# Kernel optimization log

Measured on AMD Instinct MI355X. Metric: run time of the kernel, lower is better.

## Reference

```python
import jax, jax.numpy as jnp
import numpy as np

UAV_DIM, TASK_DIM = 32, 32
E, H, HID = 128, 4, 256
B, U, T = 16, 64, 128
ENC_H = 128  # encoder hidden width


def _mlp3(x, w0, b0, w1, b1, w2, b2):
    # Linear->ReLU->Linear->ReLU->Linear (weights stored as (in,out))
    x = jax.nn.relu(x @ w0 + b0)
    x = jax.nn.relu(x @ w1 + b1)
    return x @ w2 + b2


def setup_inputs() -> dict:
    key = jax.random.key(0)
    ks = jax.random.split(key, 20)
    s = lambda fan_in: 1.0 / np.sqrt(fan_in)
    d = {
        'uav_feat': jax.random.normal(ks[0], (B, U, UAV_DIM), jnp.float32),
        'task_feat': jax.random.normal(ks[1], (B, T, TASK_DIM), jnp.float32),
        # UAV encoder
        'uw0': jax.random.normal(ks[2], (UAV_DIM, ENC_H), jnp.float32) * s(UAV_DIM),
        'ub0': jnp.zeros((ENC_H,), jnp.float32),
        'uw1': jax.random.normal(ks[3], (ENC_H, ENC_H), jnp.float32) * s(ENC_H),
        'ub1': jnp.zeros((ENC_H,), jnp.float32),
        'uw2': jax.random.normal(ks[4], (ENC_H, E), jnp.float32) * s(ENC_H),
        'ub2': jnp.zeros((E,), jnp.float32),
        # Task encoder
        'tw0': jax.random.normal(ks[5], (TASK_DIM, ENC_H), jnp.float32) * s(TASK_DIM),
        'tb0': jnp.zeros((ENC_H,), jnp.float32),
        'tw1': jax.random.normal(ks[6], (ENC_H, ENC_H), jnp.float32) * s(ENC_H),
        'tb1': jnp.zeros((ENC_H,), jnp.float32),
        'tw2': jax.random.normal(ks[7], (ENC_H, E), jnp.float32) * s(ENC_H),
        'tb2': jnp.zeros((E,), jnp.float32),
        # head queries + fusion MLP (fw1 is the (2E,HID) first linear)
        'head_q': jax.random.normal(ks[8], (H, E), jnp.float32),
        'fw1': jax.random.normal(ks[9], (2 * E, HID), jnp.float32) * s(2 * E),
        'fb1': jnp.zeros((HID,), jnp.float32),
        'fw2': jax.random.normal(ks[10], (HID, 1), jnp.float32) * s(HID),
        'fb2': jnp.zeros((1,), jnp.float32),
    }
    return d


def reference(uav_feat, task_feat, uw0, ub0, uw1, ub1, uw2, ub2,
              tw0, tb0, tw1, tb1, tw2, tb2, head_q, fw1, fb1, fw2, fb2):
    ue = _mlp3(uav_feat, uw0, ub0, uw1, ub1, uw2, ub2)   # (B,U,E)
    te = _mlp3(task_feat, tw0, tb0, tw1, tb1, tw2, tb2)  # (B,T,E)
    # q = uav_embed + per-head query: (B,H,U,E)
    q = ue[:, None, :, :] + head_q[None, :, None, :]
    # Split cat([q,k]) @ fw1 into q@fw1[:E] + k@fw1[E:] — same math, no 2E concat
    qh = jnp.einsum('bhue,ed->bhud', q, fw1[:E])          # (B,H,U,HID)
    kh = jnp.einsum('bte,ed->btd', te, fw1[E:])           # (B,T,HID)
    pre = qh[:, :, :, None, :] + kh[:, None, None, :, :] + fb1  # (B,H,U,T,HID)
    h = jax.nn.relu(pre)
    logits = jnp.einsum('bhutd,do->bhuto', h, fw2)[..., 0] + fb2[0]  # (B,H,U,T)
    return logits
```

## Files before the change

### kernel.cpp

```cpp
#include <hip/hip_runtime.h>
#include <hip/hip_bf16.h>

#define B_ 16
#define U_ 64
#define T_ 128
#define H_ 4
#define E_ 128
#define HID_ 256

typedef _Float16 half_t;
typedef _Float16 h2 __attribute__((ext_vector_type(2)));
typedef _Float16 f16x8 __attribute__((ext_vector_type(8)));
typedef float f32x4 __attribute__((ext_vector_type(4)));

__device__ __forceinline__ h2 u2h(unsigned u){ h2 r; __builtin_memcpy(&r, &u, 4); return r; }
__device__ __forceinline__ unsigned pkh(float a, float b){
  h2 r; r.x = (_Float16)a; r.y = (_Float16)b;
  unsigned u; __builtin_memcpy(&u, &r, 4); return u;
}

__global__ __launch_bounds__(256) void prep_kernel(
  const float* __restrict__ uw0, const float* __restrict__ uw1, const float* __restrict__ uw2,
  const float* __restrict__ tw0, const float* __restrict__ tw1, const float* __restrict__ tw2,
  const float* __restrict__ fw1, const float* __restrict__ headq,
  half_t* __restrict__ u0t, half_t* __restrict__ u1t, half_t* __restrict__ u2t,
  half_t* __restrict__ t0t, half_t* __restrict__ t1t, half_t* __restrict__ t2t,
  half_t* __restrict__ f1at, half_t* __restrict__ f1bt, float* __restrict__ QhW)
{
  const int tid = threadIdx.x;
  const int b = blockIdx.x;
  if (b == 34) {
    const int n = tid;
    float acc[4] = {0.f,0.f,0.f,0.f};
    for (int e=0;e<128;e++){
      float w = fw1[e*256 + n];
      #pragma unroll
      for (int h=0;h<4;h++) acc[h] = fmaf(headq[h*128+e], w, acc[h]);
    }
    #pragma unroll
    for (int h=0;h<4;h++) QhW[h*256+n] = acc[h];
    return;
  }
  const float* src; int srcStride, row0, col0; half_t* dst; int dstStride, nOff, kOff;
  if (b < 9) {
    if (b==0){ src=uw0; row0=0;        dst=u0t; dstStride=32;  kOff=0; }
    else if (b<5){ src=uw1; row0=(b-1)*32; dst=u1t; dstStride=128; kOff=row0; }
    else { src=uw2; row0=(b-5)*32; dst=u2t; dstStride=128; kOff=row0; }
    srcStride=128; col0=0; nOff=0;
  } else if (b < 18) {
    int bb=b-9;
    if (bb==0){ src=tw0; row0=0;        dst=t0t; dstStride=32;  kOff=0; }
    else if (bb<5){ src=tw1; row0=(bb-1)*32; dst=t1t; dstStride=128; kOff=row0; }
    else { src=tw2; row0=(bb-5)*32; dst=t2t; dstStride=128; kOff=row0; }
    srcStride=128; col0=0; nOff=0;
  } else if (b < 26) {
    int idx=b-18, kc=idx&3, nc=idx>>2;
    src=fw1; srcStride=256; row0=kc*32; col0=nc*128;
    dst=f1at; dstStride=128; kOff=kc*32; nOff=col0;
  } else {
    int idx=b-26, kc=idx&3, nc=idx>>2;
    src=fw1; srcStride=256; row0=128+kc*32; col0=nc*128;
    dst=f1bt; dstStride=128; kOff=kc*32; nOff=col0;
  }
  __shared__ half_t tl[128][33];
  #pragma unroll
  for (int i=0;i<16;i++){ int idx=i*256+tid; int k=idx>>7, n=idx&127;
    tl[n][k] = (half_t)src[(row0+k)*srcStride + col0 + n]; }
  __syncthreads();
  #pragma unroll
  for (int i=0;i<16;i++){ int idx=i*256+tid; int n=idx>>5, k=idx&31;
    dst[(nOff+n)*dstStride + kOff + k] = tl[n][k]; }
}

#define PITCH 136

template<int KTILES, int NTILES, bool RELU>
__device__ __forceinline__ void layer_mfma(const half_t* __restrict__ in,
    const half_t* __restrict__ W, const float* __restrict__ bias,
    half_t* __restrict__ out, int m0, int quad, int l16)
{
  f16x8 bfrag[KTILES];
  const half_t* ip = in + (m0+l16)*PITCH + quad*8;
  #pragma unroll
  for (int kk=0;kk<KTILES;kk++) bfrag[kk] = *(const f16x8*)(ip + kk*32);
  #pragma unroll
  for (int nt=0; nt<NTILES; nt++){
    f32x4 acc = {0.f,0.f,0.f,0.f};
    const half_t* wp = W + (nt*16+l16)*PITCH + quad*8;
    #pragma unroll
    for (int kk=0;kk<KTILES;kk++){
      f16x8 a = *(const f16x8*)(wp + kk*32);
      acc = __builtin_amdgcn_mfma_f32_16x16x32_f16(a, bfrag[kk], acc, 0, 0, 0);
    }
    const int n0 = nt*16 + quad*4;
    const float4 bv = *(const float4*)(bias + n0);
    float bvr[4] = {bv.x, bv.y, bv.z, bv.w};
    union { half_t h[4]; uint2 u; } pv;
    #pragma unroll
    for (int r=0;r<4;r++){
      float x = acc[r] + bvr[r];
      if (RELU) x = fmaxf(x, 0.f);
      pv.h[r] = (half_t)x;
    }
    *(uint2*)(out + (m0+l16)*PITCH + n0) = pv.u;
  }
}

__global__ __launch_bounds__(256) void enc_mfma(
  const float* __restrict__ uav, const float* __restrict__ task,
  const float* __restrict__ ub0, const float* __restrict__ ub1, const float* __restrict__ ub2,
  const float* __restrict__ tb0, const float* __restrict__ tb1, const float* __restrict__ tb2,
  const half_t* __restrict__ u0t, const half_t* __restrict__ u1t, const half_t* __restrict__ u2t,
  const half_t* __restrict__ t0t, const half_t* __restrict__ t1t, const half_t* __restrict__ t2t,
  const half_t* __restrict__ f1at, const half_t* __restrict__ f1bt,
  float* __restrict__ ueW, half_t* __restrict__ Kg)
{
  __shared__ half_t Wb[256*PITCH];
  __shared__ half_t actA[64*PITCH];
  __shared__ half_t actB[64*PITCH];
  const int tid = threadIdx.x, lane = tid&63, wv = tid>>6;
  const int quad = lane>>4, l16 = lane&15;
  const int m0 = wv*16;
  const bool isU = blockIdx.x < 16;
  const int rows0 = (isU ? blockIdx.x : blockIdx.x - 16) * 64;
  const float* Xsrc = (isU ? uav : task) + rows0*32;
  const half_t* W0 = isU ? u0t : t0t;
  const half_t* W1 = isU ? u1t : t1t;
  const half_t* W2 = isU ? u2t : t2t;
  const half_t* W3 = isU ? f1at : f1bt;
  const float* bias0 = isU ? ub0 : tb0;
  const float* bias1 = isU ? ub1 : tb1;
  const float* bias2 = isU ? ub2 : tb2;

  {
    const int r = tid>>2, q = tid&3;
    const float4 v0 = *(const float4*)(Xsrc + r*32 + q*8);
    const float4 v1 = *(const float4*)(Xsrc + r*32 + q*8 + 4);
    half_t* d = actA + r*PITCH + q*8;
    d[0]=(half_t)v0.x; d[1]=(half_t)v0.y; d[2]=(half_t)v0.z; d[3]=(half_t)v0.w;
    d[4]=(half_t)v1.x; d[5]=(half_t)v1.y; d[6]=(half_t)v1.z; d[7]=(half_t)v1.w;
  }
  {
    const uint4* s = (const uint4*)W0;
    #pragma unroll
    for (int i=0;i<2;i++){ int idx=i*256+tid; int n=idx>>2, kc=idx&3;
      *(uint4*)(Wb + n*PITCH + kc*8) = s[idx]; }
  }
  __syncthreads();
  layer_mfma<1,8,true >(actA, Wb, bias0, actB, m0, quad, l16);
  __syncthreads();
  { const uint4* s = (const uint4*)W1;
    #pragma unroll
    for (int i=0;i<8;i++){ int idx=i*256+tid; int n=idx>>4, kc=idx&15;
      *(uint4*)(Wb + n*PITCH + kc*8) = s[idx]; } }
  __syncthreads();
  layer_mfma<4,8,true >(actB, Wb, bias1, actA, m0, quad, l16);
  __syncthreads();
  { const uint4* s = (const uint4*)W2;
    #pragma unroll
    for (int i=0;i<8;i++){ int idx=i*256+tid; int n=idx>>4, kc=idx&15;
      *(uint4*)(Wb + n*PITCH + kc*8) = s[idx]; } }
  __syncthreads();
  layer_mfma<4,8,false>(actA, Wb, bias2, actB, m0, quad, l16);
  __syncthreads();
  { const uint4* s = (const uint4*)W3;
    #pragma unroll
    for (int i=0;i<16;i++){ int idx=i*256+tid; int n=idx>>4, kc=idx&15;
      *(uint4*)(Wb + n*PITCH + kc*8) = s[idx]; } }
  __syncthreads();
  {
    f16x8 bfrag[4];
    const half_t* ip = actB + (m0+l16)*PITCH + quad*8;
    #pragma unroll
    for (int kk=0;kk<4;kk++) bfrag[kk] = *(const f16x8*)(ip + kk*32);
    const int grow = rows0 + m0 + l16;
    #pragma unroll
    for (int nt=0; nt<16; nt++){
      f32x4 acc = {0.f,0.f,0.f,0.f};
      const half_t* wp = Wb + (nt*16+l16)*PITCH + quad*8;
      #pragma unroll
      for (int kk=0;kk<4;kk++){
        f16x8 a = *(const f16x8*)(wp + kk*32);
        acc = __builtin_amdgcn_mfma_f32_16x16x32_f16(a, bfrag[kk], acc, 0, 0, 0);
      }
      const int n0 = nt*16 + quad*4;
      if (isU){
        *(float4*)(ueW + grow*256 + n0) = make_float4(acc[0],acc[1],acc[2],acc[3]);
      } else {
        union { half_t h[4]; uint2 u; } pv;
        pv.h[0]=(half_t)acc[0]; pv.h[1]=(half_t)acc[1];
        pv.h[2]=(half_t)acc[2]; pv.h[3]=(half_t)acc[3];
        *(uint2*)(Kg + grow*256 + n0) = pv.u;
      }
    }
  }
}

#define UTILE 8

__global__ __launch_bounds__(256) void logits_kernel(
  const float* __restrict__ ueW, const float* __restrict__ QhW,
  const half_t* __restrict__ Kg,
  const float* __restrict__ fb1, const float* __restrict__ fw2,
  const float* __restrict__ fb2, float* __restrict__ out)
{
  __shared__ uint4 Kl4[64*32];
  __shared__ uint4 baseb[UTILE][32];
  __shared__ uint4 w2b[32];

  const int tid = threadIdx.x;
  const int wv = tid >> 6;
  const int lane = tid & 63;
  const int b = blockIdx.z, h = blockIdx.y;
  const int u0 = blockIdx.x * UTILE;

  {
    const int u = tid >> 5;
    const int c = tid & 31;
    const float4* ue4 = (const float4*)(ueW + (b*U_ + u0 + u)*HID_);
    const float4* q4  = (const float4*)(QhW + h*HID_);
    const float4* f4  = (const float4*)fb1;
    float4 a0 = ue4[2*c],   a1 = ue4[2*c+1];
    float4 b0 = q4[2*c],    b1 = q4[2*c+1];
    float4 c0 = f4[2*c],    c1 = f4[2*c+1];
    uint4 pv;
    pv.x = pkh(a0.x+b0.x+c0.x, a0.y+b0.y+c0.y);
    pv.y = pkh(a0.z+b0.z+c0.z, a0.w+b0.w+c0.w);
    pv.z = pkh(a1.x+b1.x+c1.x, a1.y+b1.y+c1.y);
    pv.w = pkh(a1.z+b1.z+c1.z, a1.w+b1.w+c1.w);
    baseb[u][c] = pv;
    if (tid < 32) {
      const float4* w4 = (const float4*)fw2;
      float4 w0 = w4[2*tid], w1 = w4[2*tid+1];
      uint4 wv4;
      wv4.x = pkh(w0.x, w0.y); wv4.y = pkh(w0.z, w0.w);
      wv4.z = pkh(w1.x, w1.y); wv4.w = pkh(w1.z, w1.w);
      w2b[tid] = wv4;
    }
  }
  const float fb2f = fb2[0];
  const uint4* Kgp = (const uint4*)(Kg + (size_t)b*T_*HID_);

  const int r0 = wv*2;
  const h2 hz = (h2)((_Float16)0);

  for (int s=0; s<2; s++){
    const int t0 = s*64;
    if (s) __syncthreads();
    for (int i = tid; i < 64*32; i += 256){
      const int t = i >> 5, c = i & 31;
      Kl4[t*32 + ((c + t)&31)] = Kgp[(t0 + t)*32 + c];
    }
    __syncthreads();
    const uint4* myrow = Kl4 + lane*32;
    float acc0 = 0.f, acc1 = 0.f;
    #pragma unroll
    for (int c=0; c<32; c++){
      const uint4 kv = myrow[(c + lane)&31];
      const uint4 w4 = w2b[c];
      const uint4 p0 = baseb[r0][c];
      const uint4 p1 = baseb[r0+1][c];
      h2 x;
      x = __builtin_elementwise_max(u2h(p0.x)+u2h(kv.x), hz);
      acc0 = __builtin_amdgcn_fdot2(x, u2h(w4.x), acc0, false);
      x = __builtin_elementwise_max(u2h(p0.y)+u2h(kv.y), hz);
      acc0 = __builtin_amdgcn_fdot2(x, u2h(w4.y), acc0, false);
      x = __builtin_elementwise_max(u2h(p0.z)+u2h(kv.z), hz);
      acc0 = __builtin_amdgcn_fdot2(x, u2h(w4.z), acc0, false);
      x = __builtin_elementwise_max(u2h(p0.w)+u2h(kv.w), hz);
      acc0 = __builtin_amdgcn_fdot2(x, u2h(w4.w), acc0, false);
      x = __builtin_elementwise_max(u2h(p1.x)+u2h(kv.x), hz);
      acc1 = __builtin_amdgcn_fdot2(x, u2h(w4.x), acc1, false);
      x = __builtin_elementwise_max(u2h(p1.y)+u2h(kv.y), hz);
      acc1 = __builtin_amdgcn_fdot2(x, u2h(w4.y), acc1, false);
      x = __builtin_elementwise_max(u2h(p1.z)+u2h(kv.z), hz);
      acc1 = __builtin_amdgcn_fdot2(x, u2h(w4.z), acc1, false);
      x = __builtin_elementwise_max(u2h(p1.w)+u2h(kv.w), hz);
      acc1 = __builtin_amdgcn_fdot2(x, u2h(w4.w), acc1, false);
    }
    const int t = t0 + lane;
    out[((b*H_ + h)*U_ + (u0 + r0    ))*T_ + t] = acc0 + fb2f;
    out[((b*H_ + h)*U_ + (u0 + r0 + 1))*T_ + t] = acc1 + fb2f;
  }
}

extern "C" void kernel_launch(void* const* d_in, const int* in_sizes, int n_in,
                              void* d_out, int out_size, void* d_ws, size_t ws_size,
                              hipStream_t stream)
{
  const float* uav  = (const float*)d_in[0];
  const float* task = (const float*)d_in[1];
  const float* uw0=(const float*)d_in[2];  const float* ub0=(const float*)d_in[3];
  const float* uw1=(const float*)d_in[4];  const float* ub1=(const float*)d_in[5];
  const float* uw2=(const float*)d_in[6];  const float* ub2=(const float*)d_in[7];
  const float* tw0=(const float*)d_in[8];  const float* tb0=(const float*)d_in[9];
  const float* tw1=(const float*)d_in[10]; const float* tb1=(const float*)d_in[11];
  const float* tw2=(const float*)d_in[12]; const float* tb2=(const float*)d_in[13];
  const float* headq=(const float*)d_in[14];
  const float* fw1=(const float*)d_in[15];
  const float* fb1=(const float*)d_in[16];
  const float* fw2=(const float*)d_in[17];
  const float* fb2=(const float*)d_in[18];

  float* ueW = (float*)d_ws;
  float* QhW = ueW + 262144;
  half_t* hb = (half_t*)(QhW + 1024);
  half_t* u0t  = hb;
  half_t* u1t  = hb + 4096;
  half_t* u2t  = hb + 20480;
  half_t* t0t  = hb + 36864;
  half_t* t1t  = hb + 40960;
  half_t* t2t  = hb + 57344;
  half_t* f1at = hb + 73728;
  half_t* f1bt = hb + 106496;
  half_t* Kg   = hb + 139264;

  float* out = (float*)d_out;

  hipLaunchKernelGGL(prep_kernel, dim3(35), dim3(256), 0, stream,
      uw0, uw1, uw2, tw0, tw1, tw2, fw1, headq,
      u0t, u1t, u2t, t0t, t1t, t2t, f1at, f1bt, QhW);
  hipLaunchKernelGGL(enc_mfma, dim3(48), dim3(256), 0, stream,
      uav, task, ub0, ub1, ub2, tb0, tb1, tb2,
      u0t, u1t, u2t, t0t, t1t, t2t, f1at, f1bt, ueW, Kg);
  hipLaunchKernelGGL(logits_kernel, dim3(U_/UTILE, H_, B_), dim3(256), 0, stream,
      ueW, QhW, Kg, fb1, fw2, fb2, out);
}
```

Baseline: 116.1 us.

## Fuse weight prep into encoder kernel and restructure logits tiling

Removes the separate weight-transpose/convert prep kernel; the encoder now reads the fp32 weights directly, converts them to fp16 while staging into shared memory, and computes QhW in an extra block. Weight staging for later layers is overlapped with MFMA compute through fewer barriers and separate buffers. The logits kernel now loads all 128 task rows of K into shared memory at once, and each thread computes 4 u-rows instead of 2 across two passes. The cost is more LDS per block, which may lower occupancy, and strided uncoalesced fp32 weight reads in every encoder block.

```diff
diff --git a/kernel.cpp b/kernel.cpp
--- a/kernel.cpp
+++ b/kernel.cpp
@@ -19,17 +19,76 @@
   unsigned u; __builtin_memcpy(&u, &r, 4); return u;
 }
 
-__global__ __launch_bounds__(256) void prep_kernel(
-  const float* __restrict__ uw0, const float* __restrict__ uw1, const float* __restrict__ uw2,
-  const float* __restrict__ tw0, const float* __restrict__ tw1, const float* __restrict__ tw2,
-  const float* __restrict__ fw1, const float* __restrict__ headq,
-  half_t* __restrict__ u0t, half_t* __restrict__ u1t, half_t* __restrict__ u2t,
-  half_t* __restrict__ t0t, half_t* __restrict__ t1t, half_t* __restrict__ t2t,
-  half_t* __restrict__ f1at, half_t* __restrict__ f1bt, float* __restrict__ QhW)
-{
+#define PITCH 136
+#define PITCH0 40
+
+template<int KC, int SRCN>
+__device__ __forceinline__ void stageW(const float* __restrict__ src,
+    half_t* __restrict__ dst, int n, int kc0, int pitch)
+{
+  #pragma unroll
+  for (int f=0; f<KC; f++){
+    const int kc = kc0 + f;
+    float v[8];
+    #pragma unroll
+    for (int j=0;j<8;j++) v[j] = src[(kc*8+j)*SRCN + n];
+    union{ half_t h[8]; uint4 u; } p;
+    #pragma unroll
+    for (int j=0;j<8;j++) p.h[j] = (half_t)v[j];
+    *(uint4*)(dst + n*pitch + kc*8) = p.u;
+  }
+}
+
+template<int KTILES, int NTILES, int WPITCH, bool RELU>
+__device__ __forceinline__ void layer_mfma(const half_t* __restrict__ in,
+    const half_t* __restrict__ W, const float* __restrict__ bias,
+    half_t* __restrict__ out, int m0, int quad, int l16)
+{
+  f16x8 bfrag[KTILES];
+  const half_t* ip = in + (m0+l16)*PITCH + quad*8;
+  #pragma unroll
+  for (int kk=0;kk<KTILES;kk++) bfrag[kk] = *(const f16x8*)(ip + kk*32);
+  #pragma unroll
+  for (int nt=0; nt<NTILES; nt++){
+    f32x4 acc = {0.f,0.f,0.f,0.f};
+    const half_t* wp = W + (nt*16+l16)*WPITCH + quad*8;
+    #pragma unroll
+    for (int kk=0;kk<KTILES;kk++){
+      f16x8 a = *(const f16x8*)(wp + kk*32);
+      acc = __builtin_amdgcn_mfma_f32_16x16x32_f16(a, bfrag[kk], acc, 0, 0, 0);
+    }
+    const int n0 = nt*16 + quad*4;
+    const float4 bv = *(const float4*)(bias + n0);
+    float bvr[4] = {bv.x, bv.y, bv.z, bv.w};
+    union { half_t h[4]; uint2 u; } pv;
+    #pragma unroll
+    for (int r=0;r<4;r++){
+      float x = acc[r] + bvr[r];
+      if (RELU) x = fmaxf(x, 0.f);
+      pv.h[r] = (half_t)x;
+    }
+    *(uint2*)(out + (m0+l16)*PITCH + n0) = pv.u;
+  }
+}
+
+__global__ __launch_bounds__(256) void enc_mfma(
+  const float* __restrict__ uav, const float* __restrict__ task,
+  const float* __restrict__ uw0, const float* __restrict__ ub0,
+  const float* __restrict__ uw1, const float* __restrict__ ub1,
+  const float* __restrict__ uw2, const float* __restrict__ ub2,
+  const float* __restrict__ tw0, const float* __restrict__ tb0,
+  const float* __restrict__ tw1, const float* __restrict__ tb1,
+  const float* __restrict__ tw2, const float* __restrict__ tb2,
+  const float* __restrict__ headq, const float* __restrict__ fw1,
+  float* __restrict__ ueW, half_t* __restrict__ Kg, float* __restrict__ QhW)
+{
+  __shared__ half_t W0b[128*PITCH0];
+  __shared__ half_t Wb[256*PITCH];
+  __shared__ half_t actA[64*PITCH];
+  __shared__ half_t actB[64*PITCH];
   const int tid = threadIdx.x;
-  const int b = blockIdx.x;
-  if (b == 34) {
+
+  if (blockIdx.x == 48) {
     const int n = tid;
     float acc[4] = {0.f,0.f,0.f,0.f};
     for (int e=0;e<128;e++){
@@ -41,133 +100,46 @@
     for (int h=0;h<4;h++) QhW[h*256+n] = acc[h];
     return;
   }
-  const float* src; int srcStride, row0, col0; half_t* dst; int dstStride, nOff, kOff;
-  if (b < 9) {
-    if (b==0){ src=uw0; row0=0;        dst=u0t; dstStride=32;  kOff=0; }
-    else if (b<5){ src=uw1; row0=(b-1)*32; dst=u1t; dstStride=128; kOff=row0; }
-    else { src=uw2; row0=(b-5)*32; dst=u2t; dstStride=128; kOff=row0; }
-    srcStride=128; col0=0; nOff=0;
-  } else if (b < 18) {
-    int bb=b-9;
-    if (bb==0){ src=tw0; row0=0;        dst=t0t; dstStride=32;  kOff=0; }
-    else if (bb<5){ src=tw1; row0=(bb-1)*32; dst=t1t; dstStride=128; kOff=row0; }
-    else { src=tw2; row0=(bb-5)*32; dst=t2t; dstStride=128; kOff=row0; }
-    srcStride=128; col0=0; nOff=0;
-  } else if (b < 26) {
-    int idx=b-18, kc=idx&3, nc=idx>>2;
-    src=fw1; srcStride=256; row0=kc*32; col0=nc*128;
-    dst=f1at; dstStride=128; kOff=kc*32; nOff=col0;
-  } else {
-    int idx=b-26, kc=idx&3, nc=idx>>2;
-    src=fw1; srcStride=256; row0=128+kc*32; col0=nc*128;
-    dst=f1bt; dstStride=128; kOff=kc*32; nOff=col0;
-  }
-  __shared__ half_t tl[128][33];
-  #pragma unroll
-  for (int i=0;i<16;i++){ int idx=i*256+tid; int k=idx>>7, n=idx&127;
-    tl[n][k] = (half_t)src[(row0+k)*srcStride + col0 + n]; }
-  __syncthreads();
-  #pragma unroll
-  for (int i=0;i<16;i++){ int idx=i*256+tid; int n=idx>>5, k=idx&31;
-    dst[(nOff+n)*dstStride + kOff + k] = tl[n][k]; }
-}
-
-#define PITCH 136
-
-template<int KTILES, int NTILES, bool RELU>
-__device__ __forceinline__ void layer_mfma(const half_t* __restrict__ in,
-    const half_t* __restrict__ W, const float* __restrict__ bias,
-    half_t* __restrict__ out, int m0, int quad, int l16)
-{
-  f16x8 bfrag[KTILES];
-  const half_t* ip = in + (m0+l16)*PITCH + quad*8;
-  #pragma unroll
-  for (int kk=0;kk<KTILES;kk++) bfrag[kk] = *(const f16x8*)(ip + kk*32);
-  #pragma unroll
-  for (int nt=0; nt<NTILES; nt++){
-    f32x4 acc = {0.f,0.f,0.f,0.f};
-    const half_t* wp = W + (nt*16+l16)*PITCH + quad*8;
-    #pragma unroll
-    for (int kk=0;kk<KTILES;kk++){
-      f16x8 a = *(const f16x8*)(wp + kk*32);
-      acc = __builtin_amdgcn_mfma_f32_16x16x32_f16(a, bfrag[kk], acc, 0, 0, 0);
-    }
-    const int n0 = nt*16 + quad*4;
-    const float4 bv = *(const float4*)(bias + n0);
-    float bvr[4] = {bv.x, bv.y, bv.z, bv.w};
-    union { half_t h[4]; uint2 u; } pv;
-    #pragma unroll
-    for (int r=0;r<4;r++){
-      float x = acc[r] + bvr[r];
-      if (RELU) x = fmaxf(x, 0.f);
-      pv.h[r] = (half_t)x;
-    }
-    *(uint2*)(out + (m0+l16)*PITCH + n0) = pv.u;
-  }
-}
-
-__global__ __launch_bounds__(256) void enc_mfma(
-  const float* __restrict__ uav, const float* __restrict__ task,
-  const float* __restrict__ ub0, const float* __restrict__ ub1, const float* __restrict__ ub2,
-  const float* __restrict__ tb0, const float* __restrict__ tb1, const float* __restrict__ tb2,
-  const half_t* __restrict__ u0t, const half_t* __restrict__ u1t, const half_t* __restrict__ u2t,
-  const half_t* __restrict__ t0t, const half_t* __restrict__ t1t, const half_t* __restrict__ t2t,
-  const half_t* __restrict__ f1at, const half_t* __restrict__ f1bt,
-  float* __restrict__ ueW, half_t* __restrict__ Kg)
-{
-  __shared__ half_t Wb[256*PITCH];
-  __shared__ half_t actA[64*PITCH];
-  __shared__ half_t actB[64*PITCH];
-  const int tid = threadIdx.x, lane = tid&63, wv = tid>>6;
+
+  const int lane = tid&63, wv = tid>>6;
   const int quad = lane>>4, l16 = lane&15;
   const int m0 = wv*16;
   const bool isU = blockIdx.x < 16;
   const int rows0 = (isU ? blockIdx.x : blockIdx.x - 16) * 64;
   const float* Xsrc = (isU ? uav : task) + rows0*32;
-  const half_t* W0 = isU ? u0t : t0t;
-  const half_t* W1 = isU ? u1t : t1t;
-  const half_t* W2 = isU ? u2t : t2t;
-  const half_t* W3 = isU ? f1at : f1bt;
+  const float* W0 = isU ? uw0 : tw0;
+  const float* W1 = isU ? uw1 : tw1;
+  const float* W2 = isU ? uw2 : tw2;
+  const float* W3 = fw1 + (isU ? 0 : 128*HID_);
   const float* bias0 = isU ? ub0 : tb0;
   const float* bias1 = isU ? ub1 : tb1;
   const float* bias2 = isU ? ub2 : tb2;
+
+  const int tn = tid & 127, th = tid >> 7;
 
   {
     const int r = tid>>2, q = tid&3;
     const float4 v0 = *(const float4*)(Xsrc + r*32 + q*8);
     const float4 v1 = *(const float4*)(Xsrc + r*32 + q*8 + 4);
-    half_t* d = actA + r*PITCH + q*8;
-    d[0]=(half_t)v0.x; d[1]=(half_t)v0.y; d[2]=(half_t)v0.z; d[3]=(half_t)v0.w;
-    d[4]=(half_t)v1.x; d[5]=(half_t)v1.y; d[6]=(half_t)v1.z; d[7]=(half_t)v1.w;
-  }
-  {
-    const uint4* s = (const uint4*)W0;
-    #pragma unroll
-    for (int i=0;i<2;i++){ int idx=i*256+tid; int n=idx>>2, kc=idx&3;
-      *(uint4*)(Wb + n*PITCH + kc*8) = s[idx]; }
-  }
-  __syncthreads();
-  layer_mfma<1,8,true >(actA, Wb, bias0, actB, m0, quad, l16);
-  __syncthreads();
-  { const uint4* s = (const uint4*)W1;
-    #pragma unroll
-    for (int i=0;i<8;i++){ int idx=i*256+tid; int n=idx>>4, kc=idx&15;
-      *(uint4*)(Wb + n*PITCH + kc*8) = s[idx]; } }
-  __syncthreads();
-  layer_mfma<4,8,true >(actB, Wb, bias1, actA, m0, quad, l16);
-  __syncthreads();
-  { const uint4* s = (const uint4*)W2;
-    #pragma unroll
-    for (int i=0;i<8;i++){ int idx=i*256+tid; int n=idx>>4, kc=idx&15;
-      *(uint4*)(Wb + n*PITCH + kc*8) = s[idx]; } }
-  __syncthreads();
-  layer_mfma<4,8,false>(actA, Wb, bias2, actB, m0, quad, l16);
-  __syncthreads();
-  { const uint4* s = (const uint4*)W3;
-    #pragma unroll
-    for (int i=0;i<16;i++){ int idx=i*256+tid; int n=idx>>4, kc=idx&15;
-      *(uint4*)(Wb + n*PITCH + kc*8) = s[idx]; } }
-  __syncthreads();
+    union{ half_t h[8]; uint4 u; } p;
+    p.h[0]=(half_t)v0.x; p.h[1]=(half_t)v0.y; p.h[2]=(half_t)v0.z; p.h[3]=(half_t)v0.w;
+    p.h[4]=(half_t)v1.x; p.h[5]=(half_t)v1.y; p.h[6]=(half_t)v1.z; p.h[7]=(half_t)v1.w;
+    *(uint4*)(actA + r*PITCH + q*8) = p.u;
+  }
+  stageW<2,128>(W0, W0b, tn, th*2, PITCH0);
+  stageW<8,128>(W1, Wb,            tn, th*8, PITCH);
+  stageW<8,128>(W2, Wb + 128*PITCH,tn, th*8, PITCH);
+  __syncthreads();
+
+  layer_mfma<1,8,PITCH0,true >(actA, W0b,          bias0, actB, m0, quad, l16);
+  layer_mfma<4,8,PITCH, true >(actB, Wb,           bias1, actA, m0, quad, l16);
+  __syncthreads();
+  stageW<8,256>(W3, Wb, tn, th*8, PITCH);
+  layer_mfma<4,8,PITCH, false>(actA, Wb+128*PITCH, bias2, actB, m0, quad, l16);
+  __syncthreads();
+  stageW<8,256>(W3, Wb, 128 + tn, th*8, PITCH);
+  __syncthreads();
+
   {
     f16x8 bfrag[4];
     const half_t* ip = actB + (m0+l16)*PITCH + quad*8;
@@ -204,13 +176,11 @@
   const float* __restrict__ fb1, const float* __restrict__ fw2,
   const float* __restrict__ fb2, float* __restrict__ out)
 {
-  __shared__ uint4 Kl4[64*32];
+  __shared__ uint4 Kl4[128*32];
   __shared__ uint4 baseb[UTILE][32];
   __shared__ uint4 w2b[32];
 
   const int tid = threadIdx.x;
-  const int wv = tid >> 6;
-  const int lane = tid & 63;
   const int b = blockIdx.z, h = blockIdx.y;
   const int u0 = blockIdx.x * UTILE;
 
@@ -238,50 +208,43 @@
       w2b[tid] = wv4;
     }
   }
+  const uint4* Kgp = (const uint4*)(Kg + (size_t)b*T_*HID_);
+  #pragma unroll
+  for (int i = tid; i < 128*32; i += 256){
+    const int t = i >> 5, c = i & 31;
+    Kl4[t*32 + ((c + t)&31)] = Kgp[t*32 + c];
+  }
+  __syncthreads();
+
+  const int wv = tid >> 6, lane = tid & 63;
+  const int r0 = (wv & 1) * 4;
+  const int t  = (wv >> 1) * 64 + lane;
   const float fb2f = fb2[0];
-  const uint4* Kgp = (const uint4*)(Kg + (size_t)b*T_*HID_);
-
-  const int r0 = wv*2;
+  const uint4* myrow = Kl4 + t*32;
   const h2 hz = (h2)((_Float16)0);
 
-  for (int s=0; s<2; s++){
-    const int t0 = s*64;
-    if (s) __syncthreads();
-    for (int i = tid; i < 64*32; i += 256){
-      const int t = i >> 5, c = i & 31;
-      Kl4[t*32 + ((c + t)&31)] = Kgp[(t0 + t)*32 + c];
-    }
-    __syncthreads();
-    const uint4* myrow = Kl4 + lane*32;
-    float acc0 = 0.f, acc1 = 0.f;
-    #pragma unroll
-    for (int c=0; c<32; c++){
-      const uint4 kv = myrow[(c + lane)&31];
-      const uint4 w4 = w2b[c];
-      const uint4 p0 = baseb[r0][c];
-      const uint4 p1 = baseb[r0+1][c];
+  float acc[4] = {0.f,0.f,0.f,0.f};
+  #pragma unroll
+  for (int c=0; c<32; c++){
+    const uint4 kv = myrow[(c + t)&31];
+    const uint4 w4 = w2b[c];
+    #pragma unroll
+    for (int r=0; r<4; r++){
+      const uint4 p = baseb[r0+r][c];
       h2 x;
-      x = __builtin_elementwise_max(u2h(p0.x)+u2h(kv.x), hz);
-      acc0 = __builtin_amdgcn_fdot2(x, u2h(w4.x), acc0, false);
-      x = __builtin_elementwise_max(u2h(p0.y)+u2h(kv.y), hz);
-      acc0 = __builtin_amdgcn_fdot2(x, u2h(w4.y), acc0, false);
-      x = __builtin_elementwise_max(u2h(p0.z)+u2h(kv.z), hz);
-      acc0 = __builtin_amdgcn_fdot2(x, u2h(w4.z), acc0, false);
-      x = __builtin_elementwise_max(u2h(p0.w)+u2h(kv.w), hz);
-      acc0 = __builtin_amdgcn_fdot2(x, u2h(w4.w), acc0, false);
-      x = __builtin_elementwise_max(u2h(p1.x)+u2h(kv.x), hz);
-      acc1 = __builtin_amdgcn_fdot2(x, u2h(w4.x), acc1, false);
-      x = __builtin_elementwise_max(u2h(p1.y)+u2h(kv.y), hz);
-      acc1 = __builtin_amdgcn_fdot2(x, u2h(w4.y), acc1, false);
-      x = __builtin_elementwise_max(u2h(p1.z)+u2h(kv.z), hz);
-      acc1 = __builtin_amdgcn_fdot2(x, u2h(w4.z), acc1, false);
-      x = __builtin_elementwise_max(u2h(p1.w)+u2h(kv.w), hz);
-      acc1 = __builtin_amdgcn_fdot2(x, u2h(w4.w), acc1, false);
-    }
-    const int t = t0 + lane;
-    out[((b*H_ + h)*U_ + (u0 + r0    ))*T_ + t] = acc0 + fb2f;
-    out[((b*H_ + h)*U_ + (u0 + r0 + 1))*T_ + t] = acc1 + fb2f;
-  }
+      x = __builtin_elementwise_max(u2h(p.x)+u2h(kv.x), hz);
+      acc[r] = __builtin_amdgcn_fdot2(x, u2h(w4.x), acc[r], false);
+      x = __builtin_elementwise_max(u2h(p.y)+u2h(kv.y), hz);
+      acc[r] = __builtin_amdgcn_fdot2(x, u2h(w4.y), acc[r], false);
+      x = __builtin_elementwise_max(u2h(p.z)+u2h(kv.z), hz);
+      acc[r] = __builtin_amdgcn_fdot2(x, u2h(w4.z), acc[r], false);
+      x = __builtin_elementwise_max(u2h(p.w)+u2h(kv.w), hz);
+      acc[r] = __builtin_amdgcn_fdot2(x, u2h(w4.w), acc[r], false);
+    }
+  }
+  #pragma unroll
+  for (int r=0; r<4; r++)
+    out[((b*H_ + h)*U_ + (u0 + r0 + r))*T_ + t] = acc[r] + fb2f;
 }
 
 extern "C" void kernel_launch(void* const* d_in, const int* in_sizes, int n_in,
@@ -304,25 +267,14 @@
 
   float* ueW = (float*)d_ws;
   float* QhW = ueW + 262144;
-  half_t* hb = (half_t*)(QhW + 1024);
-  half_t* u0t  = hb;
-  half_t* u1t  = hb + 4096;
-  half_t* u2t  = hb + 20480;
-  half_t* t0t  = hb + 36864;
-  half_t* t1t  = hb + 40960;
-  half_t* t2t  = hb + 57344;
-  half_t* f1at = hb + 73728;
-  half_t* f1bt = hb + 106496;
-  half_t* Kg   = hb + 139264;
+  half_t* Kg = (half_t*)(QhW + 1024);
 
   float* out = (float*)d_out;
 
-  hipLaunchKernelGGL(prep_kernel, dim3(35), dim3(256), 0, stream,
-      uw0, uw1, uw2, tw0, tw1, tw2, fw1, headq,
-      u0t, u1t, u2t, t0t, t1t, t2t, f1at, f1bt, QhW);
-  hipLaunchKernelGGL(enc_mfma, dim3(48), dim3(256), 0, stream,
-      uav, task, ub0, ub1, ub2, tb0, tb1, tb2,
-      u0t, u1t, u2t, t0t, t1t, t2t, f1at, f1bt, ueW, Kg);
+  hipLaunchKernelGGL(enc_mfma, dim3(49), dim3(256), 0, stream,
+      uav, task, uw0, ub0, uw1, ub1, uw2, ub2,
+      tw0, tb0, tw1, tb1, tw2, tb2, headq, fw1,
+      ueW, Kg, QhW);
   hipLaunchKernelGGL(logits_kernel, dim3(U_/UTILE, H_, B_), dim3(256), 0, stream,
       ueW, QhW, Kg, fb1, fw2, fb2, out);
 }
```

Result: faster. 113.3 us (-2.5%).
